# Kernel tuning notes

Measured on AMD Instinct MI355X. Metric: run time of the kernel, lower is better.

Reference implementation:

```python
import jax, jax.numpy as jnp
import numpy as np

N_NODES = 100000


def _gcn_conv(x, W, b, src, dst, num_nodes):
    """PyG GCNConv: h = x @ W; symmetric-normalized scatter-add over edges
    (self-loops already included in src/dst); out = aggregate + b."""
    h = x @ W  # [N, out]
    ones = jnp.ones(src.shape[0], dtype=x.dtype)
    deg = jax.ops.segment_sum(ones, dst, num_segments=num_nodes)  # in-degree incl self-loop
    dinv = jnp.where(deg > 0, jax.lax.rsqrt(deg), 0.0)
    norm = dinv[src] * dinv[dst]  # [E]
    msg = h[src] * norm[:, None]  # [E, out] -- dominant memory traffic
    out = jax.ops.segment_sum(msg, dst, num_segments=num_nodes)
    return out + b


def setup_inputs() -> dict:
    key = jax.random.key(0)
    k = jax.random.split(key, 4)
    in_c, hid, out_c = 128, 64, 32
    n_edges = 1600000
    x = jax.random.normal(k[0], (N_NODES, in_c), dtype=jnp.float32)
    edge_index = jax.random.randint(k[1], (2, n_edges), 0, N_NODES, dtype=jnp.int64)
    W1 = jax.random.normal(k[2], (in_c, hid), dtype=jnp.float32) * (1.0 / np.sqrt(in_c))
    b1 = jnp.zeros((hid,), dtype=jnp.float32)
    W2 = jax.random.normal(k[3], (hid, out_c), dtype=jnp.float32) * (1.0 / np.sqrt(hid))
    b2 = jnp.zeros((out_c,), dtype=jnp.float32)
    return {"x": x, "edge_index": edge_index, "W1": W1, "b1": b1, "W2": W2, "b2": b2}


def reference(x, edge_index, W1, b1, W2, b2):
    num_nodes = x.shape[0]
    loops = jnp.arange(num_nodes, dtype=edge_index.dtype)
    src = jnp.concatenate([edge_index[0], loops])  # add self-loops once, shared by both layers
    dst = jnp.concatenate([edge_index[1], loops])
    h = _gcn_conv(x, W1, b1, src, dst, num_nodes)
    h = jax.nn.relu(h)
    out = _gcn_conv(h, W2, b2, src, dst, num_nodes)
    return out
```

## Files before the change

kernel.cpp:

```cpp
#include <hip/hip_runtime.h>


#define NBKT(n) (((n) + 127) >> 7)

__device__ inline float bf2f(unsigned short u) {
    union { unsigned int i; float f; } v;
    v.i = ((unsigned int)u) << 16;
    return v.f;
}
__device__ inline unsigned short f2bf(float f) {
    union { float f; unsigned int i; } v;
    v.f = f;
    unsigned int u = v.i;
    return (unsigned short)((u + 0x7fff + ((u >> 16) & 1)) >> 16);
}

#define BH_CHUNK 4096
__global__ void __launch_bounds__(256) bhist_kernel(
        const int* __restrict__ dst, int E, int nbk, int* __restrict__ bcnt) {
    __shared__ int cnt[NBKT(100000)];
    const int t = threadIdx.x;
    const int beg = blockIdx.x * BH_CHUNK;
    const int end = min(E, beg + BH_CHUNK);
    for (int b = t; b < nbk; b += 256) cnt[b] = 0;
    __syncthreads();
    for (int i = beg + t; i < end; i += 256) atomicAdd(&cnt[dst[i] >> 7], 1);
    __syncthreads();
    for (int b = t; b < nbk; b += 256) {
        int c = cnt[b];
        if (c) atomicAdd(&bcnt[b], c);
    }
}

__global__ void bscan_kernel(const int* __restrict__ bcnt, int nbk, int E,
                             int* __restrict__ boffs, int* __restrict__ gcursor) {
    __shared__ int s[1024];
    const int t = threadIdx.x;
    int v = (t < nbk) ? bcnt[t] : 0;
    s[t] = v;
    __syncthreads();
    for (int off = 1; off < 1024; off <<= 1) {
        int x = (t >= off) ? s[t - off] : 0;
        __syncthreads();
        s[t] += x;
        __syncthreads();
    }
    if (t < nbk) {
        int excl = s[t] - v;
        boffs[t] = excl;
        gcursor[t] = excl;
    }
    if (t == 0) boffs[nbk] = E;
}

#define BF_CHUNK 4096
__global__ void __launch_bounds__(256) binfill_kernel(
        const int* __restrict__ src, const int* __restrict__ dst, int E, int nbk,
        int* __restrict__ gcursor, int* __restrict__ entries) {
    __shared__ int cnt[NBKT(100000)];
    __shared__ int gbase[NBKT(100000)];
    __shared__ int rank[NBKT(100000)];
    const int t = threadIdx.x;
    const int beg = blockIdx.x * BF_CHUNK;
    const int end = min(E, beg + BF_CHUNK);
    for (int b = t; b < nbk; b += 256) cnt[b] = 0;
    __syncthreads();
    for (int i = beg + t; i < end; i += 256) atomicAdd(&cnt[dst[i] >> 7], 1);
    __syncthreads();
    for (int b = t; b < nbk; b += 256) {
        int c = cnt[b];
        gbase[b] = c ? atomicAdd(&gcursor[b], c) : 0;
        rank[b] = 0;
    }
    __syncthreads();
    for (int i = beg + t; i < end; i += 256) {
        int d = dst[i];
        int b = d >> 7;
        int r = atomicAdd(&rank[b], 1);
        entries[gbase[b] + r] = (src[i] << 7) | (d & 127);
    }
}

__global__ void __launch_bounds__(256) bucket2csr_kernel(
        const int* __restrict__ entries, const int* __restrict__ boffs, int nbk,
        int* __restrict__ offs, int* __restrict__ csr_src, float* __restrict__ dinv,
        int N, int E) {
    __shared__ int cnt[128];
    __shared__ int s[128];
    __shared__ int rank[128];
    const int t = threadIdx.x;
    const int b = blockIdx.x;
    const int beg = boffs[b];
    const int end = boffs[b + 1];
    if (t < 128) { cnt[t] = 0; rank[t] = 0; }
    __syncthreads();
    for (int i = beg + t; i < end; i += 256) atomicAdd(&cnt[entries[i] & 127], 1);
    __syncthreads();
    if (t < 128) s[t] = cnt[t];
    __syncthreads();
    for (int off = 1; off < 128; off <<= 1) {
        int x = 0;
        if (t < 128 && t >= off) x = s[t - off];
        __syncthreads();
        if (t < 128) s[t] += x;
        __syncthreads();
    }
    const int node0 = b * 128;
    if (t < 128 && node0 + t < N) {
        offs[node0 + t] = beg + s[t] - cnt[t];
        dinv[node0 + t] = rsqrtf((float)cnt[t] + 1.0f);
    }
    if (b == 0 && t == 0) offs[N] = E;
    __syncthreads();
    for (int i = beg + t; i < end; i += 256) {
        int e = entries[i];
        int d = e & 127;
        int r = atomicAdd(&rank[d], 1);
        csr_src[beg + s[d] - cnt[d] + r] = (int)((unsigned)e >> 7);
    }
}

#define FMA4(ACC, AV, WV) \
    ACC.x += (AV) * (WV).x; ACC.y += (AV) * (WV).y; ACC.z += (AV) * (WV).z; ACC.w += (AV) * (WV).w;

template <int K, int C, int BR, bool BF16OUT>
__global__ void __launch_bounds__(256) gemm_tile_kernel(
        const float* __restrict__ A, const float* __restrict__ W,
        const float* __restrict__ dinv, void* __restrict__ outv, int N) {
    constexpr int F4R = K / 4;
    constexpr int CG = C / 4;
    static_assert(256 / CG * 4 == BR, "geometry");
    __shared__ float Wl[K * C];
    __shared__ float Al[BR * K];

    const int t = threadIdx.x;
    for (int i = t; i < K * C / 4; i += 256) ((float4*)Wl)[i] = ((const float4*)W)[i];
    const int row0 = blockIdx.x * BR;
    for (int i = t; i < BR * F4R; i += 256) {
        int r = i / F4R, k4 = i % F4R;
        float4 v = make_float4(0.f, 0.f, 0.f, 0.f);
        if (row0 + r < N) v = ((const float4*)(A + (size_t)(row0 + r) * K))[k4];
        *(float4*)(Al + r * K + k4 * 4) = v;
    }
    __syncthreads();

    const int c0 = (t % CG) * 4;
    const int r0 = (t / CG) * 4;
    const float* Ab = Al + r0 * K;

    float4 acc0 = {0, 0, 0, 0}, acc1 = {0, 0, 0, 0}, acc2 = {0, 0, 0, 0}, acc3 = {0, 0, 0, 0};

#pragma unroll 2
    for (int k4 = 0; k4 < K / 4; ++k4) {
        float4 a0 = *(const float4*)(Ab + 0 * K + k4 * 4);
        float4 a1 = *(const float4*)(Ab + 1 * K + k4 * 4);
        float4 a2 = *(const float4*)(Ab + 2 * K + k4 * 4);
        float4 a3 = *(const float4*)(Ab + 3 * K + k4 * 4);
        float4 w0 = *(const float4*)(Wl + (k4 * 4 + 0) * C + c0);
        float4 w1 = *(const float4*)(Wl + (k4 * 4 + 1) * C + c0);
        float4 w2 = *(const float4*)(Wl + (k4 * 4 + 2) * C + c0);
        float4 w3 = *(const float4*)(Wl + (k4 * 4 + 3) * C + c0);
        FMA4(acc0, a0.x, w0) FMA4(acc1, a1.x, w0) FMA4(acc2, a2.x, w0) FMA4(acc3, a3.x, w0)
        FMA4(acc0, a0.y, w1) FMA4(acc1, a1.y, w1) FMA4(acc2, a2.y, w1) FMA4(acc3, a3.y, w1)
        FMA4(acc0, a0.z, w2) FMA4(acc1, a1.z, w2) FMA4(acc2, a2.z, w2) FMA4(acc3, a3.z, w2)
        FMA4(acc0, a0.w, w3) FMA4(acc1, a1.w, w3) FMA4(acc2, a2.w, w3) FMA4(acc3, a3.w, w3)
    }

    const int row = row0 + r0;
#pragma unroll
    for (int i = 0; i < 4; ++i) {
        int rr = row + i;
        if (rr < N) {
            float d = dinv[rr];
            float4 fr = (i == 0) ? acc0 : (i == 1) ? acc1 : (i == 2) ? acc2 : acc3;
            fr.x *= d; fr.y *= d; fr.z *= d; fr.w *= d;
            if (BF16OUT) {
                ushort4 o;
                o.x = f2bf(fr.x); o.y = f2bf(fr.y); o.z = f2bf(fr.z); o.w = f2bf(fr.w);
                *(ushort4*)((unsigned short*)outv + (size_t)rr * C + c0) = o;
            } else {
                *(float4*)((float*)outv + (size_t)rr * C + c0) = fr;
            }
        }
    }
}

#define G64_LOAD(SS) bf2f(hs[(size_t)(SS) * 64 + lane])
template <bool RELU>
__global__ void __launch_bounds__(256) gather64_kernel(
        const unsigned short* __restrict__ hs, const float* __restrict__ dinv,
        const int* __restrict__ offs, const int* __restrict__ csr_src,
        const float* __restrict__ b, float* __restrict__ out, int N) {
    const int lane = threadIdx.x & 63;
    const int d = blockIdx.x * 4 + (threadIdx.x >> 6);
    if (d >= N) return;
    const int beg = offs[d];
    const int end = offs[d + 1];
    float acc0 = G64_LOAD(d);
    float acc1 = 0.f, acc2 = 0.f, acc3 = 0.f;
    int j = beg;
    for (; j + 15 < end; j += 16) {
        int s0 = csr_src[j + 0], s1 = csr_src[j + 1], s2 = csr_src[j + 2], s3 = csr_src[j + 3];
        int s4 = csr_src[j + 4], s5 = csr_src[j + 5], s6 = csr_src[j + 6], s7 = csr_src[j + 7];
        int s8 = csr_src[j + 8], s9 = csr_src[j + 9], sa = csr_src[j + 10], sb = csr_src[j + 11];
        int sc = csr_src[j + 12], sd = csr_src[j + 13], se = csr_src[j + 14], sf = csr_src[j + 15];
        float v0 = G64_LOAD(s0), v1 = G64_LOAD(s1), v2 = G64_LOAD(s2), v3 = G64_LOAD(s3);
        float v4 = G64_LOAD(s4), v5 = G64_LOAD(s5), v6 = G64_LOAD(s6), v7 = G64_LOAD(s7);
        float v8 = G64_LOAD(s8), v9 = G64_LOAD(s9), va = G64_LOAD(sa), vb = G64_LOAD(sb);
        float vc = G64_LOAD(sc), vd = G64_LOAD(sd), ve = G64_LOAD(se), vf = G64_LOAD(sf);
        acc0 += v0; acc1 += v1; acc2 += v2; acc3 += v3;
        acc0 += v4; acc1 += v5; acc2 += v6; acc3 += v7;
        acc0 += v8; acc1 += v9; acc2 += va; acc3 += vb;
        acc0 += vc; acc1 += vd; acc2 += ve; acc3 += vf;
    }
    if (j + 7 < end) {
        int s0 = csr_src[j + 0], s1 = csr_src[j + 1], s2 = csr_src[j + 2], s3 = csr_src[j + 3];
        int s4 = csr_src[j + 4], s5 = csr_src[j + 5], s6 = csr_src[j + 6], s7 = csr_src[j + 7];
        float v0 = G64_LOAD(s0), v1 = G64_LOAD(s1), v2 = G64_LOAD(s2), v3 = G64_LOAD(s3);
        float v4 = G64_LOAD(s4), v5 = G64_LOAD(s5), v6 = G64_LOAD(s6), v7 = G64_LOAD(s7);
        acc0 += v0; acc1 += v1; acc2 += v2; acc3 += v3;
        acc0 += v4; acc1 += v5; acc2 += v6; acc3 += v7;
        j += 8;
    }
    if (j + 3 < end) {
        int s0 = csr_src[j + 0], s1 = csr_src[j + 1], s2 = csr_src[j + 2], s3 = csr_src[j + 3];
        acc0 += G64_LOAD(s0); acc1 += G64_LOAD(s1); acc2 += G64_LOAD(s2); acc3 += G64_LOAD(s3);
        j += 4;
    }
    for (; j < end; ++j) acc0 += G64_LOAD(csr_src[j]);
    float r = ((acc0 + acc1) + (acc2 + acc3)) * dinv[d] + b[lane];
    if (RELU) r = fmaxf(r, 0.f);
    out[(size_t)d * 64 + lane] = r;
}

#define G32_LOAD(SS) bf2f(hs[(size_t)(SS) * 32 + lane])
__global__ void __launch_bounds__(256) gather32_kernel(
        const unsigned short* __restrict__ hs, const float* __restrict__ dinv,
        const int* __restrict__ offs, const int* __restrict__ csr_src,
        const float* __restrict__ b, float* __restrict__ out, int N) {
    const int lane = threadIdx.x & 31;
    const int d = blockIdx.x * 8 + (threadIdx.x >> 5);
    if (d >= N) return;
    const int beg = offs[d];
    const int end = offs[d + 1];
    float acc0 = G32_LOAD(d);
    float acc1 = 0.f, acc2 = 0.f, acc3 = 0.f;
    int j = beg;
    for (; j + 15 < end; j += 16) {
        int s0 = csr_src[j + 0], s1 = csr_src[j + 1], s2 = csr_src[j + 2], s3 = csr_src[j + 3];
        int s4 = csr_src[j + 4], s5 = csr_src[j + 5], s6 = csr_src[j + 6], s7 = csr_src[j + 7];
        int s8 = csr_src[j + 8], s9 = csr_src[j + 9], sa = csr_src[j + 10], sb = csr_src[j + 11];
        int sc = csr_src[j + 12], sd = csr_src[j + 13], se = csr_src[j + 14], sf = csr_src[j + 15];
        float v0 = G32_LOAD(s0), v1 = G32_LOAD(s1), v2 = G32_LOAD(s2), v3 = G32_LOAD(s3);
        float v4 = G32_LOAD(s4), v5 = G32_LOAD(s5), v6 = G32_LOAD(s6), v7 = G32_LOAD(s7);
        float v8 = G32_LOAD(s8), v9 = G32_LOAD(s9), va = G32_LOAD(sa), vb = G32_LOAD(sb);
        float vc = G32_LOAD(sc), vd = G32_LOAD(sd), ve = G32_LOAD(se), vf = G32_LOAD(sf);
        acc0 += v0; acc1 += v1; acc2 += v2; acc3 += v3;
        acc0 += v4; acc1 += v5; acc2 += v6; acc3 += v7;
        acc0 += v8; acc1 += v9; acc2 += va; acc3 += vb;
        acc0 += vc; acc1 += vd; acc2 += ve; acc3 += vf;
    }
    if (j + 7 < end) {
        int s0 = csr_src[j + 0], s1 = csr_src[j + 1], s2 = csr_src[j + 2], s3 = csr_src[j + 3];
        int s4 = csr_src[j + 4], s5 = csr_src[j + 5], s6 = csr_src[j + 6], s7 = csr_src[j + 7];
        float v0 = G32_LOAD(s0), v1 = G32_LOAD(s1), v2 = G32_LOAD(s2), v3 = G32_LOAD(s3);
        float v4 = G32_LOAD(s4), v5 = G32_LOAD(s5), v6 = G32_LOAD(s6), v7 = G32_LOAD(s7);
        acc0 += v0; acc1 += v1; acc2 += v2; acc3 += v3;
        acc0 += v4; acc1 += v5; acc2 += v6; acc3 += v7;
        j += 8;
    }
    if (j + 3 < end) {
        int s0 = csr_src[j + 0], s1 = csr_src[j + 1], s2 = csr_src[j + 2], s3 = csr_src[j + 3];
        acc0 += G32_LOAD(s0); acc1 += G32_LOAD(s1); acc2 += G32_LOAD(s2); acc3 += G32_LOAD(s3);
        j += 4;
    }
    for (; j < end; ++j) acc0 += G32_LOAD(csr_src[j]);
    float r = ((acc0 + acc1) + (acc2 + acc3)) * dinv[d] + b[lane];
    out[(size_t)d * 32 + lane] = r;
}

extern "C" void kernel_launch(void* const* d_in, const int* in_sizes, int n_in,
                              void* d_out, int out_size, void* d_ws, size_t ws_size,
                              hipStream_t stream) {
    const float* x = (const float*)d_in[0];
    const int* ei = (const int*)d_in[1];
    const float* W1 = (const float*)d_in[2];
    const float* b1 = (const float*)d_in[3];
    const float* W2 = (const float*)d_in[4];
    const float* b2 = (const float*)d_in[5];

    const int N = in_sizes[0] / 128;
    const int E = in_sizes[1] / 2;
    const int* src = ei;
    const int* dst = ei + E;
    const int nbk = NBKT(N);

    int* bcnt = (int*)d_ws;
    int* boffs = bcnt + 1024;
    int* gcursor = boffs + 1024;
    float* dinv = (float*)(gcursor + 1024);
    int* offs = (int*)(dinv + ((N + 255) & ~255));
    int* entries = offs + ((N + 1 + 255) & ~255);
    int* csr_src = entries + ((E + 255) & ~255);
    unsigned short* h1s = (unsigned short*)(csr_src + ((E + 255) & ~255));
    float* h2 = (float*)(h1s + (size_t)N * 64);
    unsigned short* h3s = h1s;
    float* out = (float*)d_out;

    hipMemsetAsync(bcnt, 0, 1024 * 4, stream);
    bhist_kernel<<<(E + BH_CHUNK - 1) / BH_CHUNK, 256, 0, stream>>>(dst, E, nbk, bcnt);
    bscan_kernel<<<1, 1024, 0, stream>>>(bcnt, nbk, E, boffs, gcursor);

    binfill_kernel<<<(E + BF_CHUNK - 1) / BF_CHUNK, 256, 0, stream>>>(src, dst, E, nbk, gcursor, entries);
    bucket2csr_kernel<<<nbk, 256, 0, stream>>>(entries, boffs, nbk, offs, csr_src, dinv, N, E);

    gemm_tile_kernel<128, 64, 64, true><<<(N + 63) / 64, 256, 0, stream>>>(x, W1, dinv, h1s, N);

    gather64_kernel<true><<<(N + 3) / 4, 256, 0, stream>>>(h1s, dinv, offs, csr_src, b1, h2, N);

    gemm_tile_kernel<64, 32, 128, true><<<(N + 127) / 128, 256, 0, stream>>>(h2, W2, dinv, h3s, N);

    gather32_kernel<<<(N + 7) / 8, 256, 0, stream>>>(h3s, dinv, offs, csr_src, b2, out, N);
}
```

Before: 202.8 us.

## Fuse layer-2 GEMM into layer-1 gather epilogue via wavefront shuffles

The second-layer dense transform is folded into the first-layer gather kernel. Each 64-lane wavefront computes its node's ReLU hidden row, broadcasts it with shuffles and multiplies by W2 columns held in registers, then writes the bf16 pre-scaled h3 row directly. This removes the fp32 h2 round trip through memory and one kernel launch. In exchange each thread keeps 32 W2 values in registers and does 32 shuffles per node, which raises register pressure and may lower occupancy of the latency-bound gather.

```diff
diff --git a/kernel.cpp b/kernel.cpp
--- a/kernel.cpp
+++ b/kernel.cpp
@@ -186,14 +186,20 @@
 }
 
 #define G64_LOAD(SS) bf2f(hs[(size_t)(SS) * 64 + lane])
-template <bool RELU>
-__global__ void __launch_bounds__(256) gather64_kernel(
+__global__ void __launch_bounds__(256) gather64_gemm2_kernel(
         const unsigned short* __restrict__ hs, const float* __restrict__ dinv,
         const int* __restrict__ offs, const int* __restrict__ csr_src,
-        const float* __restrict__ b, float* __restrict__ out, int N) {
+        const float* __restrict__ b1, const float* __restrict__ W2,
+        unsigned short* __restrict__ h3s, int N) {
     const int lane = threadIdx.x & 63;
     const int d = blockIdx.x * 4 + (threadIdx.x >> 6);
     if (d >= N) return;
+    const int hf = lane >> 5;
+    const int c = lane & 31;
+    float w2r[32];
+#pragma unroll
+    for (int k = 0; k < 32; ++k) w2r[k] = W2[(hf * 32 + k) * 32 + c];
+
     const int beg = offs[d];
     const int end = offs[d + 1];
     float acc0 = G64_LOAD(d);
@@ -228,9 +234,18 @@
         j += 4;
     }
     for (; j < end; ++j) acc0 += G64_LOAD(csr_src[j]);
-    float r = ((acc0 + acc1) + (acc2 + acc3)) * dinv[d] + b[lane];
-    if (RELU) r = fmaxf(r, 0.f);
-    out[(size_t)d * 64 + lane] = r;
+
+    const float dv = dinv[d];
+    float h2v = fmaxf(((acc0 + acc1) + (acc2 + acc3)) * dv + b1[lane], 0.f);
+
+    float sum = 0.f;
+#pragma unroll
+    for (int k = 0; k < 32; ++k) {
+        float hv = __shfl(h2v, hf * 32 + k);
+        sum += hv * w2r[k];
+    }
+    sum += __shfl_xor(sum, 32);
+    if (lane < 32) h3s[(size_t)d * 32 + c] = f2bf(sum * dv);
 }
 
 #define G32_LOAD(SS) bf2f(hs[(size_t)(SS) * 32 + lane])
@@ -303,8 +318,7 @@
     int* entries = offs + ((N + 1 + 255) & ~255);
     int* csr_src = entries + ((E + 255) & ~255);
     unsigned short* h1s = (unsigned short*)(csr_src + ((E + 255) & ~255));
-    float* h2 = (float*)(h1s + (size_t)N * 64);
-    unsigned short* h3s = h1s;
+    unsigned short* h3s = h1s + (size_t)N * 64;
     float* out = (float*)d_out;
 
     hipMemsetAsync(bcnt, 0, 1024 * 4, stream);
@@ -316,9 +330,7 @@
 
     gemm_tile_kernel<128, 64, 64, true><<<(N + 63) / 64, 256, 0, stream>>>(x, W1, dinv, h1s, N);
 
-    gather64_kernel<true><<<(N + 3) / 4, 256, 0, stream>>>(h1s, dinv, offs, csr_src, b1, h2, N);
-
-    gemm_tile_kernel<64, 32, 128, true><<<(N + 127) / 128, 256, 0, stream>>>(h2, W2, dinv, h3s, N);
+    gather64_gemm2_kernel<<<(N + 3) / 4, 256, 0, stream>>>(h1s, dinv, offs, csr_src, b1, W2, h3s, N);
 
     gather32_kernel<<<(N + 7) / 8, 256, 0, stream>>>(h3s, dinv, offs, csr_src, b2, out, N);
 }
```

Measured after the change: 220.7 us. +8.8%, slower.
